# Kernel tuning notes

Hardware: AMD Instinct MI355X
Metric: run time of the kernel (lower is better)

## Reference

```python
import jax, jax.numpy as jnp
import numpy as np

EPS = 1e-5
EMBED_DIM = 1024
CTX_DIM = 768
NUM_HEADS = 16
DH = EMBED_DIM // NUM_HEADS
# Faithful to torch source: embed_dim // num_heads ** 0.5 parses as embed_dim // (num_heads**0.5)
SCALE = EMBED_DIM // (NUM_HEADS ** 0.5)  # = 256.0


def ws_conv1x1(x, w, b, mask):
    # weight-standardized 1x1 conv1d: w [O, I, 1], x [B, I, T]
    w2 = w[..., 0]
    mu = jnp.mean(w2, axis=1, keepdims=True)
    var = jnp.var(w2, axis=1, keepdims=True)
    wn = (w2 - mu) * jax.lax.rsqrt(var + EPS)
    y = jnp.einsum('oi,bit->bot', wn, x) + b[None, :, None]
    if mask is not None:
        y = jnp.where(mask, y, 0.0)  # mask [B,1,T] bool
    return y


def layernorm(x, g, b):
    # normalize over last axis
    mu = jnp.mean(x, axis=-1, keepdims=True)
    var = jnp.var(x, axis=-1, keepdims=True)
    return (x - mu) * jax.lax.rsqrt(var + EPS) * g + b


def setup_inputs() -> dict:
    key = jax.random.key(0)
    ks = jax.random.split(key, 16)
    B, T, S = 4, 1024, 1024
    inp = {
        'x': jax.random.normal(ks[0], (B, EMBED_DIM, T), dtype=jnp.float32),
        'context': jax.random.normal(ks[1], (B, CTX_DIM, S), dtype=jnp.float32),
        'mask': jax.random.randint(ks[2], (B, 1, T), 0, 2).astype(bool),
        'mask_ctx': jax.random.randint(ks[3], (B, 1, S), 0, 2).astype(bool),
        'qw': jax.random.normal(ks[4], (EMBED_DIM, EMBED_DIM, 1), dtype=jnp.float32) * 0.02,
        'qb': jnp.zeros((EMBED_DIM,), jnp.float32),
        'kw': jax.random.normal(ks[5], (EMBED_DIM, CTX_DIM, 1), dtype=jnp.float32) * 0.02,
        'kb': jnp.zeros((EMBED_DIM,), jnp.float32),
        'vw': jax.random.normal(ks[6], (EMBED_DIM, CTX_DIM, 1), dtype=jnp.float32) * 0.02,
        'vb': jnp.zeros((EMBED_DIM,), jnp.float32),
        'ow': jax.random.normal(ks[7], (EMBED_DIM, EMBED_DIM, 1), dtype=jnp.float32) * 0.02,
        'ob': jnp.zeros((EMBED_DIM,), jnp.float32),
        'gq': jnp.ones((DH,), jnp.float32), 'bq': jnp.zeros((DH,), jnp.float32),
        'gk': jnp.ones((DH,), jnp.float32), 'bk': jnp.zeros((DH,), jnp.float32),
        'gv': jnp.ones((DH,), jnp.float32), 'bv': jnp.zeros((DH,), jnp.float32),
    }
    return inp


def reference(x, context, mask, mask_ctx, qw, qb, kw, kb, vw, vb, ow, ob, gq, bq, gk, bk, gv, bv):
    B, E, T = x.shape
    S = context.shape[-1]
    q = ws_conv1x1(x, qw, qb, mask)            # [B,E,T]
    k = ws_conv1x1(context, kw, kb, mask_ctx)  # [B,E,S]
    v = ws_conv1x1(context, vw, vb, mask_ctx)  # [B,E,S]
    # split heads -> [B,H,dh,L]
    q = q.reshape(B, NUM_HEADS, DH, T)
    k = k.reshape(B, NUM_HEADS, DH, S)
    v = v.reshape(B, NUM_HEADS, DH, S)
    # middle_norm: LayerNorm over dh (applied on transposed layout)
    q = jnp.swapaxes(layernorm(jnp.swapaxes(q, -1, -2), gq, bq), -1, -2)
    k = jnp.swapaxes(layernorm(jnp.swapaxes(k, -1, -2), gk, bk), -1, -2)
    v = jnp.swapaxes(layernorm(jnp.swapaxes(v, -1, -2), gv, bv), -1, -2)
    # scores: k^T @ q -> [B,H,S,T]
    scores = jnp.einsum('bhds,bhdt->bhst', k, q) / SCALE
    scores = jnp.where(mask[:, :, None, :], scores, -1e9)  # mask over query dim T
    scores = jax.nn.softmax(scores, axis=-1)               # softmax over T (as in source)
    scores = jnp.where(mask_ctx[:, :, :, None], scores, 0.0)
    out = jnp.einsum('bhds,bhst->bhdt', v, scores)          # v @ scores -> [B,H,dh,T]
    out = out.reshape(B, E, T)
    out = ws_conv1x1(out, ow, ob, mask) + x
    return out
```

## Files before the change

kernel.cpp:

```cpp
#include <hip/hip_runtime.h>

#define NB 4
#define TT 1024
#define SS 1024
#define EE 1024
#define CCH 768
#define NH 16
#define DHH 64
#define EPSF 1e-5f
#define QSCALE (1.4426950408889634f / 256.0f)

typedef unsigned short u16;
typedef __attribute__((ext_vector_type(8))) short short8;
typedef __attribute__((ext_vector_type(8))) unsigned short u16x8;
typedef __attribute__((ext_vector_type(4))) unsigned short u16x4;
typedef __attribute__((ext_vector_type(4))) float f32x4;

__device__ __forceinline__ u16 f2bu(float f) {
    union { float f; unsigned u; } x; x.f = f;
    unsigned r = x.u + 0x7fffu + ((x.u >> 16) & 1u);
    return (u16)(r >> 16);
}
__device__ __forceinline__ float bu2f(u16 u) {
    union { unsigned u; float f; } x; x.u = ((unsigned)u) << 16; return x.f;
}

#if __has_builtin(__builtin_amdgcn_exp2f)
#define EXP2(x) __builtin_amdgcn_exp2f(x)
#else
#define EXP2(x) exp2f(x)
#endif

#define MFMA16(a, b, c) __builtin_amdgcn_mfma_f32_16x16x32_bf16((a), (b), (c), 0, 0, 0)

#define PREP_WS_END   4096
#define PREP_SCAN_END (PREP_WS_END + 8)
#define PREP_TR_END   (PREP_SCAN_END + 1792)
#define PREP_FILL_END (PREP_TR_END + 4096)

__global__ __launch_bounds__(256) void prep(
    const float* __restrict__ qw, const float* __restrict__ kw,
    const float* __restrict__ vw, const float* __restrict__ ow,
    u16* __restrict__ wqn, u16* __restrict__ wkn,
    u16* __restrict__ wvn, u16* __restrict__ won,
    const float* __restrict__ x, const float* __restrict__ ctx,
    const int* __restrict__ mask, const int* __restrict__ mask_ctx,
    u16* __restrict__ xc, u16* __restrict__ cc,
    int* __restrict__ tIdx, int* __restrict__ sIdx,
    int* __restrict__ cntQ, int* __restrict__ cntK,
    float* __restrict__ outF) {
    __shared__ float tile[64][65];
    __shared__ int spos[64], smask[64], wtoti[4];
    __shared__ float sa[4], sb2[4], smean, srstd;
    int bid = blockIdx.x, tid = threadIdx.x;

    if (bid < PREP_WS_END) {
        int mat = bid >> 10, row = bid & 1023;
        const float* w = mat == 0 ? qw : (mat == 1 ? kw : (mat == 2 ? vw : ow));
        u16* wn = mat == 0 ? wqn : (mat == 1 ? wkn : (mat == 2 ? wvn : won));
        int I = (mat == 1 || mat == 2) ? CCH : EE;
        const float* wr = w + (size_t)row * I;
        float s = 0.f, s2 = 0.f;
        for (int i = tid; i < I; i += 256) { float v = wr[i]; s += v; s2 += v * v; }
#pragma unroll
        for (int off = 32; off > 0; off >>= 1) { s += __shfl_down(s, off); s2 += __shfl_down(s2, off); }
        int wid = tid >> 6;
        if ((tid & 63) == 0) { sa[wid] = s; sb2[wid] = s2; }
        __syncthreads();
        if (tid == 0) {
            float ts = sa[0] + sa[1] + sa[2] + sa[3];
            float ts2 = sb2[0] + sb2[1] + sb2[2] + sb2[3];
            float mean = ts / (float)I;
            float var = ts2 / (float)I - mean * mean;
            smean = mean; srstd = rsqrtf(var + EPSF);
        }
        __syncthreads();
        float mean = smean, r = srstd;
        u16* wo = wn + (size_t)row * I;
        for (int i = tid; i < I; i += 256) wo[i] = f2bu((wr[i] - mean) * r);
        return;
    }
    if (bid < PREP_SCAN_END) {
        int t = bid - PREP_WS_END;
        int which = t & 1, b = t >> 1;
        const int* m = (which ? mask_ctx : mask) + b * 1024;
        int* idx = (which ? sIdx : tIdx) + b * 1024;
        int* cnt = (which ? cntK : cntQ) + b;
        int base = tid * 4;
        int v[4]; int s = 0;
#pragma unroll
        for (int i = 0; i < 4; i++) { v[i] = m[base + i] ? 1 : 0; s += v[i]; }
        int lane = tid & 63, wid = tid >> 6;
        int inc = s;
#pragma unroll
        for (int off = 1; off < 64; off <<= 1) {
            int o = __shfl_up(inc, off);
            if (lane >= off) inc += o;
        }
        if (lane == 63) wtoti[wid] = inc;
        __syncthreads();
        int woff = 0;
        for (int i = 0; i < wid; i++) woff += wtoti[i];
        int p = woff + inc - s;
#pragma unroll
        for (int i = 0; i < 4; i++) {
            if (v[i]) idx[p] = base + i;
            p += v[i];
        }
        if (tid == 255) *cnt = p;
        return;
    }
    if (bid < PREP_TR_END) {
        int t = bid - PREP_SCAN_END;
        int xb = t & 15; int rem = t >> 4;
        int yy = rem % 28, b = rem / 28;
        int mat = yy < 16 ? 0 : 1;
        int r0 = (mat == 0 ? yy : yy - 16) * 64;
        int R = mat == 0 ? EE : CCH;
        const float* in = mat == 0 ? x : ctx;
        const int* m = (mat == 0 ? mask : mask_ctx) + (size_t)b * 1024;
        u16* out = mat == 0 ? xc : cc;
        int c0 = xb * 64;
        const float* ip = in + (size_t)b * R * 1024;
        u16* op = out + (size_t)b * R * 1024;
#pragma unroll
        for (int mm = 0; mm < 16; mm++) {
            int id = tid + 256 * mm; int r = id >> 6, c = id & 63;
            tile[r][c] = ip[(size_t)(r0 + r) * 1024 + c0 + c];
        }
        int base = tid * 4;
        int v[4]; int s = 0;
#pragma unroll
        for (int i = 0; i < 4; i++) { v[i] = m[base + i] ? 1 : 0; s += v[i]; }
        int lane = tid & 63, wid = tid >> 6;
        int inc = s;
#pragma unroll
        for (int off = 1; off < 64; off <<= 1) {
            int o = __shfl_up(inc, off);
            if (lane >= off) inc += o;
        }
        if (lane == 63) wtoti[wid] = inc;
        __syncthreads();
        int woff = 0;
        for (int i = 0; i < wid; i++) woff += wtoti[i];
        int p = woff + inc - s;
#pragma unroll
        for (int i = 0; i < 4; i++) {
            int g = base + i;
            if (g >= c0 && g < c0 + 64) { spos[g - c0] = p; smask[g - c0] = v[i]; }
            p += v[i];
        }
        __syncthreads();
#pragma unroll
        for (int mm = 0; mm < 16; mm++) {
            int id = tid + 256 * mm; int rr = id >> 6, cc2 = id & 63;
            if (smask[rr])
                op[(size_t)spos[rr] * R + r0 + cc2] = f2bu(tile[cc2][rr]);
        }
        return;
    }
    {
        int f = bid - PREP_TR_END;
        int b = f >> 10, o = f & 1023;
        const float* xr = x + ((size_t)b * EE + o) * TT;
        float* orow = outF + ((size_t)b * EE + o) * TT;
        const int* mrow = mask + (size_t)b * TT;
        int4 mv = ((const int4*)mrow)[tid];
        float4 xv = ((const float4*)xr)[tid];
        int t4 = tid * 4;
        if (!mv.x) orow[t4 + 0] = xv.x;
        if (!mv.y) orow[t4 + 1] = xv.y;
        if (!mv.z) orow[t4 + 2] = xv.z;
        if (!mv.w) orow[t4 + 3] = xv.w;
    }
}

__device__ __forceinline__ void gemm_core(
    const u16* __restrict__ A, const u16* __restrict__ Bp, int I,
    int o0, int l0, u16 (*at)[72], u16 (*bt)[72], f32x4 (&acc)[4][2]) {
    int tid = threadIdx.x;
    int w = tid >> 6, lane = tid & 63, quad = lane >> 4, l16 = lane & 15;
    int wm = w & 1, wn = w >> 1;
    int rA = tid >> 3, cA = (tid & 7) * 8;
    u16x8 ra[2][4], rb[2][2];
#pragma unroll
    for (int p = 0; p < 2; p++) {
        int kb = p * 64;
#pragma unroll
        for (int m = 0; m < 4; m++)
            ra[p][m] = *(const u16x8*)&A[(size_t)(o0 + rA + 32 * m) * I + kb + cA];
#pragma unroll
        for (int m = 0; m < 2; m++)
            rb[p][m] = *(const u16x8*)&Bp[(size_t)(l0 + rA + 32 * m) * I + kb + cA];
    }
    for (int k0 = 0; k0 < I; k0 += 128) {
#pragma unroll
        for (int half = 0; half < 2; half++) {
            __syncthreads();
#pragma unroll
            for (int m = 0; m < 4; m++) *(u16x8*)&at[rA + 32 * m][cA] = ra[half][m];
#pragma unroll
            for (int m = 0; m < 2; m++) *(u16x8*)&bt[rA + 32 * m][cA] = rb[half][m];
            __syncthreads();
            int kpre = k0 + half * 64 + 128;
            if (kpre < I) {
#pragma unroll
                for (int m = 0; m < 4; m++)
                    ra[half][m] = *(const u16x8*)&A[(size_t)(o0 + rA + 32 * m) * I + kpre + cA];
#pragma unroll
                for (int m = 0; m < 2; m++)
                    rb[half][m] = *(const u16x8*)&Bp[(size_t)(l0 + rA + 32 * m) * I + kpre + cA];
            }
#pragma unroll
            for (int ks = 0; ks < 64; ks += 32) {
                short8 af[4], bf[2];
#pragma unroll
                for (int i = 0; i < 4; i++)
                    af[i] = *(const short8*)&at[wm * 64 + i * 16 + l16][ks + quad * 8];
#pragma unroll
                for (int j = 0; j < 2; j++)
                    bf[j] = *(const short8*)&bt[wn * 32 + j * 16 + l16][ks + quad * 8];
#pragma unroll
                for (int mt = 0; mt < 4; mt++)
#pragma unroll
                    for (int nt = 0; nt < 2; nt++)
                        acc[mt][nt] = MFMA16(af[mt], bf[nt], acc[mt][nt]);
            }
        }
    }
}

__global__ __launch_bounds__(256) void proj_qkv(
    const u16* __restrict__ wq, const u16* __restrict__ wk, const u16* __restrict__ wv,
    const u16* __restrict__ xc, const u16* __restrict__ cc,
    const float* __restrict__ qb, const float* __restrict__ kb, const float* __restrict__ vbi,
    const int* __restrict__ cntQ, const int* __restrict__ cntK,
    const float* __restrict__ gq, const float* __restrict__ bq,
    const float* __restrict__ gk, const float* __restrict__ bk,
    const float* __restrict__ gv, const float* __restrict__ bv,
    u16* __restrict__ qc, u16* __restrict__ kc, u16* __restrict__ vn) {
    int mat = blockIdx.x >> 3;
    int o0 = (blockIdx.x & 7) * 128;
    int l0 = blockIdx.y * 64;
    int b = blockIdx.z;
    int limit = (mat == 0) ? cntQ[b] : cntK[b];
    if (l0 >= limit) return;
    __shared__ u16 at[128][72];
    __shared__ u16 bt[64][72];
    __shared__ float sg[64], sbe[64], sbias[128];
    int tid = threadIdx.x;
    int w = tid >> 6, lane = tid & 63, quad = lane >> 4, l16 = lane & 15;
    int wm = w & 1, wn = w >> 1;
    const u16* A = mat == 0 ? wq : (mat == 1 ? wk : wv);
    const u16* BT = mat == 0 ? xc : cc;
    const float* bias = mat == 0 ? qb : (mat == 1 ? kb : vbi);
    int I = mat == 0 ? EE : CCH;
    if (tid < 64) {
        const float* gsrc = mat == 0 ? gq : (mat == 1 ? gk : gv);
        const float* bsrc = mat == 0 ? bq : (mat == 1 ? bk : bv);
        sg[tid] = gsrc[tid];
        sbe[tid] = bsrc[tid];
    }
    if (tid < 128) sbias[tid] = bias[o0 + tid];

    f32x4 acc[4][2] = {};
    gemm_core(A, BT + (size_t)b * 1024 * I, I, o0, l0, at, bt, acc);

    float scale = mat == 0 ? QSCALE : 1.0f;
    int h = (o0 >> 6) + wm;
    int bh = b * NH + h;
#pragma unroll
    for (int nt = 0; nt < 2; nt++) {
        int l = l0 + wn * 32 + nt * 16 + l16;
        float vbuf[16];
        float s = 0.f;
#pragma unroll
        for (int mt = 0; mt < 4; mt++)
#pragma unroll
            for (int reg = 0; reg < 4; reg++) {
                float v = acc[mt][nt][reg] + sbias[wm * 64 + mt * 16 + quad * 4 + reg];
                vbuf[mt * 4 + reg] = v; s += v;
            }
        s += __shfl_xor(s, 16); s += __shfl_xor(s, 32);
        float mean = s * (1.f / 64);
        float s2 = 0.f;
#pragma unroll
        for (int i = 0; i < 16; i++) { float dv = vbuf[i] - mean; s2 += dv * dv; }
        s2 += __shfl_xor(s2, 16); s2 += __shfl_xor(s2, 32);
        float r = rsqrtf(s2 * (1.f / 64) + EPSF);
        if (l < limit) {
            if (mat < 2) {
                u16* outT = mat == 0 ? qc : kc;
                u16* op = outT + ((size_t)bh * 1024 + l) * 64;
#pragma unroll
                for (int mt = 0; mt < 4; mt++) {
                    u16x4 pk;
#pragma unroll
                    for (int reg = 0; reg < 4; reg++) {
                        int d = mt * 16 + quad * 4 + reg;
                        pk[reg] = f2bu(((vbuf[mt * 4 + reg] - mean) * r * sg[d] + sbe[d]) * scale);
                    }
                    *(u16x4*)&op[mt * 16 + quad * 4] = pk;
                }
            } else {
#pragma unroll
                for (int mt = 0; mt < 4; mt++)
#pragma unroll
                    for (int reg = 0; reg < 4; reg++) {
                        int d = mt * 16 + quad * 4 + reg;
                        vn[((size_t)b * EE + h * 64 + d) * 1024 + l] =
                            f2bu((vbuf[mt * 4 + reg] - mean) * r * sg[d] + sbe[d]);
                    }
            }
        }
    }
}

__global__ __launch_bounds__(256) void attn_stats_mfma(
    const u16* __restrict__ qc, const u16* __restrict__ kc,
    const int* __restrict__ cntQ, const int* __restrict__ cntK,
    float* __restrict__ lneg) {
    int s0 = blockIdx.x * 64, h = blockIdx.y, b = blockIdx.z;
    int Sc = cntK[b], Tc = cntQ[b];
    if (s0 >= Sc) return;
    __shared__ u16 kt[64][72];
    __shared__ u16 qt[64][72];
    __shared__ float lp[4][64];
    int tid = threadIdx.x;
    int w = tid >> 6, lane = tid & 63, quad = lane >> 4, l16 = lane & 15;
    int head = b * NH + h;
    const u16* kp = kc + (size_t)head * SS * DHH;
    const u16* qp = qc + (size_t)head * TT * DHH;
    int rA = tid >> 3, cA = (tid & 7) * 8;
#pragma unroll
    for (int m = 0; m < 2; m++)
        *(u16x8*)&kt[rA + 32 * m][cA] = *(const u16x8*)&kp[(size_t)(s0 + rA + 32 * m) * DHH + cA];
    u16x8 rq[2][2];
#pragma unroll
    for (int p = 0; p < 2; p++)
#pragma unroll
        for (int m = 0; m < 2; m++)
            rq[p][m] = *(const u16x8*)&qp[(size_t)(p * 64 + rA + 32 * m) * DHH + cA];
    float rl[4][4] = {};
    for (int t0 = 0; t0 < Tc; t0 += 128) {
#pragma unroll
        for (int half = 0; half < 2; half++) {
            int tb = t0 + half * 64;
            __syncthreads();
#pragma unroll
            for (int m = 0; m < 2; m++) *(u16x8*)&qt[rA + 32 * m][cA] = rq[half][m];
            __syncthreads();
            int tpre = tb + 128;
            if (tpre < TT) {
#pragma unroll
                for (int m = 0; m < 2; m++)
                    rq[half][m] = *(const u16x8*)&qp[(size_t)(tpre + rA + 32 * m) * DHH + cA];
            }
            int tcol = tb + w * 16 + l16;
            f32x4 acc[4] = {};
#pragma unroll
            for (int ks = 0; ks < 64; ks += 32) {
                short8 bf = *(const short8*)&qt[w * 16 + l16][ks + quad * 8];
#pragma unroll
                for (int mt = 0; mt < 4; mt++) {
                    short8 af = *(const short8*)&kt[mt * 16 + l16][ks + quad * 8];
                    acc[mt] = MFMA16(af, bf, acc[mt]);
                }
            }
            if (tcol < Tc) {
#pragma unroll
                for (int mt = 0; mt < 4; mt++)
#pragma unroll
                    for (int reg = 0; reg < 4; reg++)
                        rl[mt][reg] += EXP2(acc[mt][reg]);
            }
        }
    }
#pragma unroll
    for (int mt = 0; mt < 4; mt++) {
#pragma unroll
        for (int reg = 0; reg < 4; reg++) {
            float v = rl[mt][reg];
            v += __shfl_xor(v, 1); v += __shfl_xor(v, 2);
            v += __shfl_xor(v, 4); v += __shfl_xor(v, 8);
            if (l16 == 0) lp[w][mt * 16 + quad * 4 + reg] = v;
        }
    }
    __syncthreads();
    if (tid < 64 && s0 + tid < Sc) {
        float lv = lp[0][tid] + lp[1][tid] + lp[2][tid] + lp[3][tid];
        lneg[(size_t)head * SS + s0 + tid] = -log2f(fmaxf(lv, 1e-30f));
    }
}

__global__ __launch_bounds__(256) void attn_pv_mfma(
    const u16* __restrict__ qc, const u16* __restrict__ kc, const u16* __restrict__ vn,
    const int* __restrict__ cntQ, const int* __restrict__ cntK,
    const float* __restrict__ lneg, u16* __restrict__ ac) {
    int t0 = blockIdx.x * 64, h = blockIdx.y, b = blockIdx.z;
    int Tc = cntQ[b], Sc = cntK[b];
    if (t0 >= Tc) return;
    __shared__ u16 qt[64][72];
    __shared__ u16 kt[64][72];
    __shared__ u16 vt[64][72];
    __shared__ u16 pt[64][72];
    __shared__ float sln[SS];
    int tid = threadIdx.x;
    int w = tid >> 6, lane = tid & 63, quad = lane >> 4, l16 = lane & 15;
    int head = b * NH + h;
    const u16* qp = qc + (size_t)head * TT * DHH;
    const u16* kp = kc + (size_t)head * SS * DHH;
    const u16* vp = vn + ((size_t)head * DHH) * SS;
    int rA = tid >> 3, cA = (tid & 7) * 8;
    for (int i = tid; i < SS; i += 256) sln[i] = lneg[(size_t)head * SS + i];
#pragma unroll
    for (int m = 0; m < 2; m++)
        *(u16x8*)&qt[rA + 32 * m][cA] = *(const u16x8*)&qp[(size_t)(t0 + rA + 32 * m) * DHH + cA];
    u16x8 rk[2][2], rv[2][2];
#pragma unroll
    for (int p = 0; p < 2; p++)
#pragma unroll
        for (int m = 0; m < 2; m++) {
            rk[p][m] = *(const u16x8*)&kp[(size_t)(p * 64 + rA + 32 * m) * DHH + cA];
            rv[p][m] = *(const u16x8*)&vp[(size_t)(rA + 32 * m) * SS + p * 64 + cA];
        }
    int tl = w * 16 + l16;

    f32x4 oacc[4] = {};
    for (int s0 = 0; s0 < Sc; s0 += 128) {
#pragma unroll
        for (int half = 0; half < 2; half++) {
            int sb = s0 + half * 64;
            if (sb >= Sc) break;
            __syncthreads();
#pragma unroll
            for (int m = 0; m < 2; m++) {
                *(u16x8*)&kt[rA + 32 * m][cA] = rk[half][m];
                *(u16x8*)&vt[rA + 32 * m][cA] = rv[half][m];
            }
            __syncthreads();
            int spre = sb + 128;
            if (spre < SS) {
#pragma unroll
                for (int m = 0; m < 2; m++) {
                    rk[half][m] = *(const u16x8*)&kp[(size_t)(spre + rA + 32 * m) * DHH + cA];
                    rv[half][m] = *(const u16x8*)&vp[(size_t)(rA + 32 * m) * SS + spre + cA];
                }
            }
            f32x4 acc[4] = {};
#pragma unroll
            for (int ks = 0; ks < 64; ks += 32) {
                short8 bf = *(const short8*)&qt[tl][ks + quad * 8];
#pragma unroll
                for (int mt = 0; mt < 4; mt++) {
                    short8 af = *(const short8*)&kt[mt * 16 + l16][ks + quad * 8];
                    acc[mt] = MFMA16(af, bf, acc[mt]);
                }
            }
#pragma unroll
            for (int mt = 0; mt < 4; mt++) {
                u16x4 pk;
#pragma unroll
                for (int reg = 0; reg < 4; reg++) {
                    int sl = mt * 16 + quad * 4 + reg;
                    pk[reg] = (sb + sl < Sc) ? f2bu(EXP2(acc[mt][reg] + sln[sb + sl])) : (u16)0;
                }
                *(u16x4*)&pt[tl][mt * 16 + quad * 4] = pk;
            }
#pragma unroll
            for (int ks = 0; ks < 64; ks += 32) {
                short8 bf = *(const short8*)&pt[tl][ks + quad * 8];
#pragma unroll
                for (int mt = 0; mt < 4; mt++) {
                    short8 af = *(const short8*)&vt[mt * 16 + l16][ks + quad * 8];
                    oacc[mt] = MFMA16(af, bf, oacc[mt]);
                }
            }
        }
    }
    __syncthreads();
#pragma unroll
    for (int mt = 0; mt < 4; mt++) {
        u16x4 pk;
#pragma unroll
        for (int reg = 0; reg < 4; reg++) pk[reg] = f2bu(oacc[mt][reg]);
        *(u16x4*)&pt[tl][mt * 16 + quad * 4] = pk;
    }
    __syncthreads();
#pragma unroll
    for (int i = 0; i < 2; i++) {
        int id = tid * 2 + i;
        int r = id >> 3, c = (id & 7) * 8;
        if (t0 + r < Tc)
            *(u16x8*)&ac[((size_t)b * TT + t0 + r) * EE + h * 64 + c] =
                *(const u16x8*)&pt[r][c];
    }
}

__global__ __launch_bounds__(256) void proj_o(
    const u16* __restrict__ won, const u16* __restrict__ ac,
    const float* __restrict__ obi, const int* __restrict__ tIdx,
    const int* __restrict__ cntQ, const float* __restrict__ x,
    float* __restrict__ out) {
    int o0 = blockIdx.x * 128, l0 = blockIdx.y * 64, b = blockIdx.z;
    int Tc = cntQ[b];
    if (l0 >= Tc) return;
    __shared__ u16 at[128][72];
    __shared__ u16 bt[64][72];
    __shared__ float sbias[128];
    __shared__ int stre[64];
    int tid = threadIdx.x;
    int w = tid >> 6, lane = tid & 63, quad = lane >> 4, l16 = lane & 15;
    int wm = w & 1, wn = w >> 1;
    if (tid < 128) sbias[tid] = obi[o0 + tid];
    if (tid < 64) stre[tid] = tIdx[(size_t)b * 1024 + l0 + tid];
    f32x4 acc[4][2] = {};
    gemm_core(won, ac + (size_t)b * TT * EE, EE, o0, l0, at, bt, acc);
#pragma unroll
    for (int nt = 0; nt < 2; nt++) {
        int lcol = wn * 32 + nt * 16 + l16;
        int l = l0 + lcol;
        if (l < Tc) {
            int treal = stre[lcol];
#pragma unroll
            for (int mt = 0; mt < 4; mt++)
#pragma unroll
                for (int reg = 0; reg < 4; reg++) {
                    int o = o0 + wm * 64 + mt * 16 + quad * 4 + reg;
                    size_t off = ((size_t)b * EE + o) * TT + treal;
                    out[off] = acc[mt][nt][reg] + sbias[wm * 64 + mt * 16 + quad * 4 + reg] + x[off];
                }
        }
    }
}

extern "C" void kernel_launch(void* const* d_in, const int* in_sizes, int n_in,
                              void* d_out, int out_size, void* d_ws, size_t ws_size,
                              hipStream_t stream) {
    const float* x        = (const float*)d_in[0];
    const float* ctx      = (const float*)d_in[1];
    const int*   mask     = (const int*)d_in[2];
    const int*   mask_ctx = (const int*)d_in[3];
    const float* qw  = (const float*)d_in[4];
    const float* qbi = (const float*)d_in[5];
    const float* kw  = (const float*)d_in[6];
    const float* kbi = (const float*)d_in[7];
    const float* vw  = (const float*)d_in[8];
    const float* vbi = (const float*)d_in[9];
    const float* ow  = (const float*)d_in[10];
    const float* obi = (const float*)d_in[11];
    const float* gq = (const float*)d_in[12];
    const float* bq = (const float*)d_in[13];
    const float* gk = (const float*)d_in[14];
    const float* bk = (const float*)d_in[15];
    const float* gv = (const float*)d_in[16];
    const float* bv = (const float*)d_in[17];

    u16* p = (u16*)d_ws;
    u16* wqn = p; p += (size_t)EE * EE;
    u16* wkn = p; p += (size_t)EE * CCH;
    u16* wvn = p; p += (size_t)EE * CCH;
    u16* won = p; p += (size_t)EE * EE;
    u16* xc  = p; p += (size_t)NB * TT * EE;
    u16* cc  = p; p += (size_t)NB * SS * CCH;
    u16* vn  = p; p += (size_t)NB * EE * SS;
    u16* qc  = p; p += (size_t)NB * NH * TT * DHH;
    u16* kc  = p; p += (size_t)NB * NH * SS * DHH;
    u16* ac  = p; p += (size_t)NB * TT * EE;
    float* lneg = (float*)p; p += (size_t)NB * NH * SS * 2;
    int* tIdx = (int*)p;
    int* sIdx = tIdx + NB * 1024;
    int* cntQ = sIdx + NB * 1024;
    int* cntK = cntQ + NB;

    prep<<<PREP_FILL_END, 256, 0, stream>>>(
        qw, kw, vw, ow, wqn, wkn, wvn, won, x, ctx, mask, mask_ctx,
        xc, cc, tIdx, sIdx, cntQ, cntK, (float*)d_out);

    proj_qkv<<<dim3(24, 16, NB), 256, 0, stream>>>(
        wqn, wkn, wvn, xc, cc, qbi, kbi, vbi, cntQ, cntK,
        gq, bq, gk, bk, gv, bv, qc, kc, vn);

    attn_stats_mfma<<<dim3(16, NH, NB), 256, 0, stream>>>(
        qc, kc, cntQ, cntK, lneg);

    attn_pv_mfma<<<dim3(16, NH, NB), 256, 0, stream>>>(
        qc, kc, vn, cntQ, cntK, lneg, ac);

    proj_o<<<dim3(8, 16, NB), 256, 0, stream>>>(
        won, ac, obi, tIdx, cntQ, x, (float*)d_out);
}
```

Baseline: 226.0 us.

## Stage GEMM and attention tiles with direct global-to-LDS loads into swizzled double buffers

Replaces the register-staged global→LDS copies in gemm_core, attn_stats_mfma and the attention-output kernel with __builtin_amdgcn_global_load_lds. Each copy moves 16 bytes per lane into an XOR-swizzled 64-column LDS tile, with two buffers per operand. This drops the padded row layout and the register round-trip, and needs one barrier per 64-wide k step instead of two per step. The next tile's loads now overlap the MFMA work on the current one. The risk is that correctness relies on the barrier also waiting for the asynchronous LDS-DMA loads to finish, and the larger double-buffered LDS footprint may lower occupancy.

Measured after the change: 229.0 us. About the same (+1.3%).

```diff
diff --git a/kernel.cpp b/kernel.cpp
--- a/kernel.cpp
+++ b/kernel.cpp
@@ -32,6 +32,31 @@
 #endif
 
 #define MFMA16(a, b, c) __builtin_amdgcn_mfma_f32_16x16x32_bf16((a), (b), (c), 0, 0, 0)
+
+__device__ __forceinline__ void gload16(const void* g, void* l) {
+    __builtin_amdgcn_global_load_lds(
+        (const __attribute__((address_space(1))) void*)g,
+        (__attribute__((address_space(3))) void*)l, 16, 0, 0);
+}
+
+template<int R>
+__device__ __forceinline__ void stage_tile(
+    const u16* __restrict__ g, int ldg, u16* lds, int w, int lane) {
+    constexpr int PW = R / 32;
+    int r0 = lane >> 3;
+    int cs = ((lane & 7) << 4) ^ (r0 << 4);
+#pragma unroll
+    for (int j = 0; j < PW; j++) {
+        int inst = w * PW + j;
+        const u16* src = g + (size_t)(inst * 8 + r0) * ldg + (cs >> 1);
+        gload16(src, lds + inst * 512);
+    }
+}
+
+__device__ __forceinline__ const u16* swz_ptr(const u16* tile, int row, int col) {
+    int off = row * 128 + ((col * 2) ^ ((row & 7) << 4));
+    return (const u16*)((const char*)tile + off);
+}
 
 #define PREP_WS_END   4096
 #define PREP_SCAN_END (PREP_WS_END + 8)
@@ -177,56 +202,38 @@
 
 __device__ __forceinline__ void gemm_core(
     const u16* __restrict__ A, const u16* __restrict__ Bp, int I,
-    int o0, int l0, u16 (*at)[72], u16 (*bt)[72], f32x4 (&acc)[4][2]) {
+    int o0, int l0, u16 (*at)[128][64], u16 (*bt)[64][64], f32x4 (&acc)[4][2]) {
     int tid = threadIdx.x;
     int w = tid >> 6, lane = tid & 63, quad = lane >> 4, l16 = lane & 15;
     int wm = w & 1, wn = w >> 1;
-    int rA = tid >> 3, cA = (tid & 7) * 8;
-    u16x8 ra[2][4], rb[2][2];
-#pragma unroll
-    for (int p = 0; p < 2; p++) {
-        int kb = p * 64;
-#pragma unroll
-        for (int m = 0; m < 4; m++)
-            ra[p][m] = *(const u16x8*)&A[(size_t)(o0 + rA + 32 * m) * I + kb + cA];
-#pragma unroll
-        for (int m = 0; m < 2; m++)
-            rb[p][m] = *(const u16x8*)&Bp[(size_t)(l0 + rA + 32 * m) * I + kb + cA];
-    }
-    for (int k0 = 0; k0 < I; k0 += 128) {
-#pragma unroll
-        for (int half = 0; half < 2; half++) {
-            __syncthreads();
-#pragma unroll
-            for (int m = 0; m < 4; m++) *(u16x8*)&at[rA + 32 * m][cA] = ra[half][m];
-#pragma unroll
-            for (int m = 0; m < 2; m++) *(u16x8*)&bt[rA + 32 * m][cA] = rb[half][m];
-            __syncthreads();
-            int kpre = k0 + half * 64 + 128;
-            if (kpre < I) {
-#pragma unroll
-                for (int m = 0; m < 4; m++)
-                    ra[half][m] = *(const u16x8*)&A[(size_t)(o0 + rA + 32 * m) * I + kpre + cA];
-#pragma unroll
-                for (int m = 0; m < 2; m++)
-                    rb[half][m] = *(const u16x8*)&Bp[(size_t)(l0 + rA + 32 * m) * I + kpre + cA];
-            }
-#pragma unroll
-            for (int ks = 0; ks < 64; ks += 32) {
-                short8 af[4], bf[2];
-#pragma unroll
-                for (int i = 0; i < 4; i++)
-                    af[i] = *(const short8*)&at[wm * 64 + i * 16 + l16][ks + quad * 8];
-#pragma unroll
-                for (int j = 0; j < 2; j++)
-                    bf[j] = *(const short8*)&bt[wn * 32 + j * 16 + l16][ks + quad * 8];
-#pragma unroll
-                for (int mt = 0; mt < 4; mt++)
-#pragma unroll
-                    for (int nt = 0; nt < 2; nt++)
-                        acc[mt][nt] = MFMA16(af[mt], bf[nt], acc[mt][nt]);
-            }
-        }
+    const u16* Ab = A + (size_t)o0 * I;
+    const u16* Bb = Bp + (size_t)l0 * I;
+    stage_tile<128>(Ab, I, &at[0][0][0], w, lane);
+    stage_tile<64>(Bb, I, &bt[0][0][0], w, lane);
+    __syncthreads();
+    int cur = 0;
+    for (int k0 = 0; k0 < I; k0 += 64, cur ^= 1) {
+        int kn = k0 + 64;
+        if (kn < I) {
+            stage_tile<128>(Ab + kn, I, &at[cur ^ 1][0][0], w, lane);
+            stage_tile<64>(Bb + kn, I, &bt[cur ^ 1][0][0], w, lane);
+        }
+#pragma unroll
+        for (int ks = 0; ks < 64; ks += 32) {
+            short8 af[4], bf[2];
+#pragma unroll
+            for (int i = 0; i < 4; i++)
+                af[i] = *(const short8*)swz_ptr(&at[cur][0][0], wm * 64 + i * 16 + l16, ks + quad * 8);
+#pragma unroll
+            for (int j = 0; j < 2; j++)
+                bf[j] = *(const short8*)swz_ptr(&bt[cur][0][0], wn * 32 + j * 16 + l16, ks + quad * 8);
+#pragma unroll
+            for (int mt = 0; mt < 4; mt++)
+#pragma unroll
+                for (int nt = 0; nt < 2; nt++)
+                    acc[mt][nt] = MFMA16(af[mt], bf[nt], acc[mt][nt]);
+        }
+        __syncthreads();
     }
 }
 
@@ -245,8 +252,8 @@
     int b = blockIdx.z;
     int limit = (mat == 0) ? cntQ[b] : cntK[b];
     if (l0 >= limit) return;
-    __shared__ u16 at[128][72];
-    __shared__ u16 bt[64][72];
+    __shared__ u16 at[2][128][64];
+    __shared__ u16 bt[2][64][64];
     __shared__ float sg[64], sbe[64], sbias[128];
     int tid = threadIdx.x;
     int w = tid >> 6, lane = tid & 63, quad = lane >> 4, l16 = lane & 15;
@@ -323,58 +330,41 @@
     int s0 = blockIdx.x * 64, h = blockIdx.y, b = blockIdx.z;
     int Sc = cntK[b], Tc = cntQ[b];
     if (s0 >= Sc) return;
-    __shared__ u16 kt[64][72];
-    __shared__ u16 qt[64][72];
+    __shared__ u16 kt[64][64];
+    __shared__ u16 qt[2][64][64];
     __shared__ float lp[4][64];
     int tid = threadIdx.x;
     int w = tid >> 6, lane = tid & 63, quad = lane >> 4, l16 = lane & 15;
     int head = b * NH + h;
     const u16* kp = kc + (size_t)head * SS * DHH;
     const u16* qp = qc + (size_t)head * TT * DHH;
-    int rA = tid >> 3, cA = (tid & 7) * 8;
-#pragma unroll
-    for (int m = 0; m < 2; m++)
-        *(u16x8*)&kt[rA + 32 * m][cA] = *(const u16x8*)&kp[(size_t)(s0 + rA + 32 * m) * DHH + cA];
-    u16x8 rq[2][2];
-#pragma unroll
-    for (int p = 0; p < 2; p++)
-#pragma unroll
-        for (int m = 0; m < 2; m++)
-            rq[p][m] = *(const u16x8*)&qp[(size_t)(p * 64 + rA + 32 * m) * DHH + cA];
+    stage_tile<64>(kp + (size_t)s0 * DHH, DHH, &kt[0][0], w, lane);
+    stage_tile<64>(qp, DHH, &qt[0][0][0], w, lane);
+    __syncthreads();
     float rl[4][4] = {};
-    for (int t0 = 0; t0 < Tc; t0 += 128) {
-#pragma unroll
-        for (int half = 0; half < 2; half++) {
-            int tb = t0 + half * 64;
-            __syncthreads();
-#pragma unroll
-            for (int m = 0; m < 2; m++) *(u16x8*)&qt[rA + 32 * m][cA] = rq[half][m];
-            __syncthreads();
-            int tpre = tb + 128;
-            if (tpre < TT) {
-#pragma unroll
-                for (int m = 0; m < 2; m++)
-                    rq[half][m] = *(const u16x8*)&qp[(size_t)(tpre + rA + 32 * m) * DHH + cA];
+    int cur = 0;
+    for (int t0 = 0; t0 < Tc; t0 += 64, cur ^= 1) {
+        if (t0 + 64 < Tc)
+            stage_tile<64>(qp + (size_t)(t0 + 64) * DHH, DHH, &qt[cur ^ 1][0][0], w, lane);
+        f32x4 acc[4] = {};
+#pragma unroll
+        for (int ks = 0; ks < 64; ks += 32) {
+            short8 bf = *(const short8*)swz_ptr(&qt[cur][0][0], w * 16 + l16, ks + quad * 8);
+#pragma unroll
+            for (int mt = 0; mt < 4; mt++) {
+                short8 af = *(const short8*)swz_ptr(&kt[0][0], mt * 16 + l16, ks + quad * 8);
+                acc[mt] = MFMA16(af, bf, acc[mt]);
             }
-            int tcol = tb + w * 16 + l16;
-            f32x4 acc[4] = {};
-#pragma unroll
-            for (int ks = 0; ks < 64; ks += 32) {
-                short8 bf = *(const short8*)&qt[w * 16 + l16][ks + quad * 8];
-#pragma unroll
-                for (int mt = 0; mt < 4; mt++) {
-                    short8 af = *(const short8*)&kt[mt * 16 + l16][ks + quad * 8];
-                    acc[mt] = MFMA16(af, bf, acc[mt]);
-                }
-            }
-            if (tcol < Tc) {
-#pragma unroll
-                for (int mt = 0; mt < 4; mt++)
-#pragma unroll
-                    for (int reg = 0; reg < 4; reg++)
-                        rl[mt][reg] += EXP2(acc[mt][reg]);
-            }
-        }
+        }
+        int tcol = t0 + w * 16 + l16;
+        if (tcol < Tc) {
+#pragma unroll
+            for (int mt = 0; mt < 4; mt++)
+#pragma unroll
+                for (int reg = 0; reg < 4; reg++)
+                    rl[mt][reg] += EXP2(acc[mt][reg]);
+        }
+        __syncthreads();
     }
 #pragma unroll
     for (int mt = 0; mt < 4; mt++) {
@@ -400,9 +390,9 @@
     int t0 = blockIdx.x * 64, h = blockIdx.y, b = blockIdx.z;
     int Tc = cntQ[b], Sc = cntK[b];
     if (t0 >= Tc) return;
-    __shared__ u16 qt[64][72];
-    __shared__ u16 kt[64][72];
-    __shared__ u16 vt[64][72];
+    __shared__ u16 qt[64][64];
+    __shared__ u16 kt[2][64][64];
+    __shared__ u16 vt[2][64][64];
     __shared__ u16 pt[64][72];
     __shared__ float sln[SS];
     int tid = threadIdx.x;
@@ -411,74 +401,51 @@
     const u16* qp = qc + (size_t)head * TT * DHH;
     const u16* kp = kc + (size_t)head * SS * DHH;
     const u16* vp = vn + ((size_t)head * DHH) * SS;
-    int rA = tid >> 3, cA = (tid & 7) * 8;
     for (int i = tid; i < SS; i += 256) sln[i] = lneg[(size_t)head * SS + i];
-#pragma unroll
-    for (int m = 0; m < 2; m++)
-        *(u16x8*)&qt[rA + 32 * m][cA] = *(const u16x8*)&qp[(size_t)(t0 + rA + 32 * m) * DHH + cA];
-    u16x8 rk[2][2], rv[2][2];
-#pragma unroll
-    for (int p = 0; p < 2; p++)
-#pragma unroll
-        for (int m = 0; m < 2; m++) {
-            rk[p][m] = *(const u16x8*)&kp[(size_t)(p * 64 + rA + 32 * m) * DHH + cA];
-            rv[p][m] = *(const u16x8*)&vp[(size_t)(rA + 32 * m) * SS + p * 64 + cA];
-        }
+    stage_tile<64>(qp + (size_t)t0 * DHH, DHH, &qt[0][0], w, lane);
+    stage_tile<64>(kp, DHH, &kt[0][0][0], w, lane);
+    stage_tile<64>(vp, SS, &vt[0][0][0], w, lane);
+    __syncthreads();
     int tl = w * 16 + l16;
-
     f32x4 oacc[4] = {};
-    for (int s0 = 0; s0 < Sc; s0 += 128) {
-#pragma unroll
-        for (int half = 0; half < 2; half++) {
-            int sb = s0 + half * 64;
-            if (sb >= Sc) break;
-            __syncthreads();
-#pragma unroll
-            for (int m = 0; m < 2; m++) {
-                *(u16x8*)&kt[rA + 32 * m][cA] = rk[half][m];
-                *(u16x8*)&vt[rA + 32 * m][cA] = rv[half][m];
+    int cur = 0;
+    for (int s0 = 0; s0 < Sc; s0 += 64, cur ^= 1) {
+        int sn = s0 + 64;
+        if (sn < Sc) {
+            stage_tile<64>(kp + (size_t)sn * DHH, DHH, &kt[cur ^ 1][0][0], w, lane);
+            stage_tile<64>(vp + sn, SS, &vt[cur ^ 1][0][0], w, lane);
+        }
+        f32x4 acc[4] = {};
+#pragma unroll
+        for (int ks = 0; ks < 64; ks += 32) {
+            short8 bf = *(const short8*)swz_ptr(&qt[0][0], tl, ks + quad * 8);
+#pragma unroll
+            for (int mt = 0; mt < 4; mt++) {
+                short8 af = *(const short8*)swz_ptr(&kt[cur][0][0], mt * 16 + l16, ks + quad * 8);
+                acc[mt] = MFMA16(af, bf, acc[mt]);
             }
-            __syncthreads();
-            int spre = sb + 128;
-            if (spre < SS) {
-#pragma unroll
-                for (int m = 0; m < 2; m++) {
-                    rk[half][m] = *(const u16x8*)&kp[(size_t)(spre + rA + 32 * m) * DHH + cA];
-                    rv[half][m] = *(const u16x8*)&vp[(size_t)(rA + 32 * m) * SS + spre + cA];
-                }
+        }
+#pragma unroll
+        for (int mt = 0; mt < 4; mt++) {
+            u16x4 pk;
+#pragma unroll
+            for (int reg = 0; reg < 4; reg++) {
+                int sl = mt * 16 + quad * 4 + reg;
+                pk[reg] = (s0 + sl < Sc) ? f2bu(EXP2(acc[mt][reg] + sln[s0 + sl])) : (u16)0;
             }
-            f32x4 acc[4] = {};
-#pragma unroll
-            for (int ks = 0; ks < 64; ks += 32) {
-                short8 bf = *(const short8*)&qt[tl][ks + quad * 8];
-#pragma unroll
-                for (int mt = 0; mt < 4; mt++) {
-                    short8 af = *(const short8*)&kt[mt * 16 + l16][ks + quad * 8];
-                    acc[mt] = MFMA16(af, bf, acc[mt]);
-                }
+            *(u16x4*)&pt[tl][mt * 16 + quad * 4] = pk;
+        }
+#pragma unroll
+        for (int ks = 0; ks < 64; ks += 32) {
+            short8 bf = *(const short8*)&pt[tl][ks + quad * 8];
+#pragma unroll
+            for (int mt = 0; mt < 4; mt++) {
+                short8 af = *(const short8*)swz_ptr(&vt[cur][0][0], mt * 16 + l16, ks + quad * 8);
+                oacc[mt] = MFMA16(af, bf, oacc[mt]);
             }
-#pragma unroll
-            for (int mt = 0; mt < 4; mt++) {
-                u16x4 pk;
-#pragma unroll
-                for (int reg = 0; reg < 4; reg++) {
-                    int sl = mt * 16 + quad * 4 + reg;
-                    pk[reg] = (sb + sl < Sc) ? f2bu(EXP2(acc[mt][reg] + sln[sb + sl])) : (u16)0;
-                }
-                *(u16x4*)&pt[tl][mt * 16 + quad * 4] = pk;
-            }
-#pragma unroll
-            for (int ks = 0; ks < 64; ks += 32) {
-                short8 bf = *(const short8*)&pt[tl][ks + quad * 8];
-#pragma unroll
-                for (int mt = 0; mt < 4; mt++) {
-                    short8 af = *(const short8*)&vt[mt * 16 + l16][ks + quad * 8];
-                    oacc[mt] = MFMA16(af, bf, oacc[mt]);
-                }
-            }
-        }
-    }
-    __syncthreads();
+        }
+        __syncthreads();
+    }
 #pragma unroll
     for (int mt = 0; mt < 4; mt++) {
         u16x4 pk;
@@ -505,8 +472,8 @@
     int o0 = blockIdx.x * 128, l0 = blockIdx.y * 64, b = blockIdx.z;
     int Tc = cntQ[b];
     if (l0 >= Tc) return;
-    __shared__ u16 at[128][72];
-    __shared__ u16 bt[64][72];
+    __shared__ u16 at[2][128][64];
+    __shared__ u16 bt[2][64][64];
     __shared__ float sbias[128];
     __shared__ int stre[64];
     int tid = threadIdx.x;
```
